# Performance work log

Measured on AMD Instinct MI355X. Metric: run time of the kernel, lower is better.

Reference implementation:

```python
import jax, jax.numpy as jnp
import numpy as np

B, S, E, H = 8, 512, 1024, 16
Dh = E // H
MAX_LEN = 512


def setup_inputs() -> dict:
    key = jax.random.key(0)
    ks = jax.random.split(key, 16)
    std = 1.0 / np.sqrt(E)
    inp = {
        "query": jax.random.normal(ks[0], (B, S, E), jnp.float32),
        "key": jax.random.normal(ks[1], (B, S, E), jnp.float32),
        "value": jax.random.normal(ks[2], (B, S, E), jnp.float32),
        "Wq": jax.random.normal(ks[3], (E, E), jnp.float32) * std,
        "bq": jax.random.normal(ks[4], (E,), jnp.float32) * std,
        "Wk": jax.random.normal(ks[5], (E, E), jnp.float32) * std,
        "bk": jax.random.normal(ks[6], (E,), jnp.float32) * std,
        "Wv": jax.random.normal(ks[7], (E, E), jnp.float32) * std,
        "bv": jax.random.normal(ks[8], (E,), jnp.float32) * std,
        "Wo": jax.random.normal(ks[9], (E, E), jnp.float32) * std,
        "bo": jax.random.normal(ks[10], (E,), jnp.float32) * std,
        "pos": jax.random.normal(ks[11], (MAX_LEN, 1, E), jnp.float32),
    }
    return inp


def reference(query, key, value, Wq, bq, Wk, bk, Wv, bv, Wo, bo, pos):
    b, sq, e = query.shape
    s = min(sq, key.shape[1])  # target_seq_length (static)
    scale = np.sqrt(Dh).astype(np.float32)
    pe = pos[:s, 0, :][None]  # [1, s, E] broadcast over batch
    q = query[:, :s] @ Wq.T + bq + pe
    k = key[:, :s] @ Wk.T + bk + pe
    v = value[:, :s] @ Wv.T + bv + pe
    # [b, s, H, Dh]
    q = q.reshape(b, s, H, Dh)
    k = k.reshape(b, s, H, Dh)
    v = v.reshape(b, s, H, Dh)
    scores = jnp.einsum("bqhd,bkhd->bhqk", q, k) / scale
    attn = jax.nn.softmax(scores, axis=-1)
    wv = jnp.einsum("bhqk,bkhd->bqhd", attn, v).reshape(b, s, e)
    return wv @ Wo.T + bo
```

## Files before the change

kernel.cpp:

```cpp
#include <hip/hip_runtime.h>
#include <hip/hip_bf16.h>

typedef __attribute__((ext_vector_type(8))) short bfx8;
typedef __attribute__((ext_vector_type(4))) float fx4;

static __device__ __forceinline__ short f2bf(float f) {
  union { float f; unsigned u; } v; v.f = f;
  unsigned r = v.u + 0x7fffu + ((v.u >> 16) & 1u);
  return (short)(r >> 16);
}

static __device__ __forceinline__ void gld16(const void* g, void* l) {
  __builtin_amdgcn_global_load_lds(
      (const __attribute__((address_space(1))) void*)g,
      (__attribute__((address_space(3))) void*)l, 16, 0, 0);
}

constexpr int Bz = 8, Sq = 512, Em = 1024, Hn = 16, Dh = 64;
constexpr int Mrows = Bz * Sq;
constexpr size_t NE = (size_t)Mrows * Em;
constexpr size_t WE = (size_t)Em * Em;

__global__ __launch_bounds__(256) void convert_kernel(
    const float* __restrict__ q, const float* __restrict__ k,
    const float* __restrict__ v,
    const float* __restrict__ Wq, const float* __restrict__ Wk,
    const float* __restrict__ Wv, const float* __restrict__ Wo,
    short* __restrict__ qx, short* __restrict__ kx, short* __restrict__ vx,
    short* __restrict__ wqb, short* __restrict__ wkb,
    short* __restrict__ wvb, short* __restrict__ wob)
{
  const int seg = blockIdx.y;
  const float* src; short* dst; size_t n;
  switch (seg) {
    case 0: src = q;  dst = qx;  n = NE; break;
    case 1: src = k;  dst = kx;  n = NE; break;
    case 2: src = v;  dst = vx;  n = NE; break;
    case 3: src = Wq; dst = wqb; n = WE; break;
    case 4: src = Wk; dst = wkb; n = WE; break;
    case 5: src = Wv; dst = wvb; n = WE; break;
    default: src = Wo; dst = wob; n = WE; break;
  }
  const size_t i = ((size_t)blockIdx.x * 256 + threadIdx.x) * 8;
  if (i >= n) return;
  fx4 a = *(const fx4*)(src + i);
  fx4 b = *(const fx4*)(src + i + 4);
  bfx8 o = { f2bf(a[0]), f2bf(a[1]), f2bf(a[2]), f2bf(a[3]),
             f2bf(b[0]), f2bf(b[1]), f2bf(b[2]), f2bf(b[3]) };
  *(bfx8*)(dst + i) = o;
}


__global__ __launch_bounds__(256) void gemm_qkv_bf16(
    const short* __restrict__ qx, const short* __restrict__ kx,
    const short* __restrict__ vx,
    const short* __restrict__ Wqb, const short* __restrict__ Wkb,
    const short* __restrict__ Wvb,
    const float* __restrict__ bq, const float* __restrict__ bk,
    const float* __restrict__ bv,
    const float* __restrict__ pos,
    short* __restrict__ qb, short* __restrict__ kb, short* __restrict__ vb)
{
  __shared__ short As[128 * 32];
  __shared__ short Bs[128 * 32];
  const int z = blockIdx.z;
  const short* A = (z == 0) ? qx : (z == 1) ? kx : vx;
  const short* W = (z == 0) ? Wqb : (z == 1) ? Wkb : Wvb;
  const float* bias = (z == 0) ? bq : (z == 1) ? bk : bv;
  short* dst = (z == 0) ? qb : (z == 1) ? kb : vb;

  const int m0 = blockIdx.x * 128, n0 = blockIdx.y * 128;
  const int t = threadIdx.x, lane = t & 63, wave = t >> 6;
  const int wr = wave >> 1, wc = wave & 1;
  const int fr = lane & 15, fq = lane >> 4;

  const int r0 = t >> 2, o0 = (t & 3) * 8;
  const int r1 = r0 + 64;
  short* lA0 = As + wave * 512;
  short* lA1 = As + 2048 + wave * 512;
  short* lB0 = Bs + wave * 512;
  short* lB1 = Bs + 2048 + wave * 512;

  fx4 acc[4][4] = {};

  for (int k0 = 0; k0 < Em; k0 += 32) {
    gld16(A + (size_t)(m0 + r0) * Em + k0 + o0, lA0);
    gld16(A + (size_t)(m0 + r1) * Em + k0 + o0, lA1);
    gld16(W + (size_t)(n0 + r0) * Em + k0 + o0, lB0);
    gld16(W + (size_t)(n0 + r1) * Em + k0 + o0, lB1);
    __syncthreads();

    bfx8 af[4], bf[4];
#pragma unroll
    for (int m = 0; m < 4; ++m)
      af[m] = *(const bfx8*)&As[(wr * 64 + m * 16 + fr) * 32 + fq * 8];
#pragma unroll
    for (int n = 0; n < 4; ++n)
      bf[n] = *(const bfx8*)&Bs[(wc * 64 + n * 16 + fr) * 32 + fq * 8];
#pragma unroll
    for (int m = 0; m < 4; ++m)
#pragma unroll
      for (int n = 0; n < 4; ++n)
        acc[m][n] = __builtin_amdgcn_mfma_f32_16x16x32_bf16(af[m], bf[n], acc[m][n], 0, 0, 0);
    __syncthreads();
  }

#pragma unroll
  for (int m = 0; m < 4; ++m) {
    const int mm = m0 + wr * 64 + m * 16 + fq * 4;
#pragma unroll
    for (int n = 0; n < 4; ++n) {
      const int nn = n0 + wc * 64 + n * 16 + fr;
      const float bb = bias[nn];
      const int h = nn >> 6, d = nn & 63;
#pragma unroll
      for (int i = 0; i < 4; ++i) {
        const int row = mm + i;
        const int s = row & (Sq - 1), b = row >> 9;
        const float val = acc[m][n][i] + bb + pos[(size_t)s * Em + nn];
        dst[(((size_t)b * Hn + h) * Sq + s) * Dh + d] = f2bf(val);
      }
    }
  }
}

__global__ __launch_bounds__(256) void gemm_out_bf16(
    const short* __restrict__ wv, const short* __restrict__ Wob,
    const float* __restrict__ bo, float* __restrict__ out)
{
  __shared__ short As[128 * 32];
  __shared__ short Bs[128 * 32];

  const int m0 = blockIdx.x * 128, n0 = blockIdx.y * 128;
  const int t = threadIdx.x, lane = t & 63, wave = t >> 6;
  const int wr = wave >> 1, wc = wave & 1;
  const int fr = lane & 15, fq = lane >> 4;

  const int r0 = t >> 2, o0 = (t & 3) * 8;
  const int r1 = r0 + 64;
  short* lA0 = As + wave * 512;
  short* lA1 = As + 2048 + wave * 512;
  short* lB0 = Bs + wave * 512;
  short* lB1 = Bs + 2048 + wave * 512;

  fx4 acc[4][4] = {};

  for (int k0 = 0; k0 < Em; k0 += 32) {
    gld16(wv + (size_t)(m0 + r0) * Em + k0 + o0, lA0);
    gld16(wv + (size_t)(m0 + r1) * Em + k0 + o0, lA1);
    gld16(Wob + (size_t)(n0 + r0) * Em + k0 + o0, lB0);
    gld16(Wob + (size_t)(n0 + r1) * Em + k0 + o0, lB1);
    __syncthreads();

    bfx8 af[4], bf[4];
#pragma unroll
    for (int m = 0; m < 4; ++m)
      af[m] = *(const bfx8*)&As[(wr * 64 + m * 16 + fr) * 32 + fq * 8];
#pragma unroll
    for (int n = 0; n < 4; ++n)
      bf[n] = *(const bfx8*)&Bs[(wc * 64 + n * 16 + fr) * 32 + fq * 8];
#pragma unroll
    for (int m = 0; m < 4; ++m)
#pragma unroll
      for (int n = 0; n < 4; ++n)
        acc[m][n] = __builtin_amdgcn_mfma_f32_16x16x32_bf16(af[m], bf[n], acc[m][n], 0, 0, 0);
    __syncthreads();
  }

#pragma unroll
  for (int m = 0; m < 4; ++m) {
    const int mm = m0 + wr * 64 + m * 16 + fq * 4;
#pragma unroll
    for (int n = 0; n < 4; ++n) {
      const int nn = n0 + wc * 64 + n * 16 + fr;
      const float bb = bo[nn];
#pragma unroll
      for (int i = 0; i < 4; ++i)
        out[(size_t)(mm + i) * Em + nn] = acc[m][n][i] + bb;
    }
  }
}

constexpr int KVB = 64, LDK = 72;

__global__ __launch_bounds__(256) void attn_kernel(
    const short* __restrict__ qb, const short* __restrict__ kb,
    const short* __restrict__ vb, short* __restrict__ wv)
{
  __shared__ short Ks[KVB * LDK];
  __shared__ short Vt[Dh * LDK];
  __shared__ short Ps[4][16 * LDK];

  const int bh = blockIdx.x;
  const int qt = blockIdx.y;
  const int t = threadIdx.x, lane = t & 63, wave = t >> 6;
  const int fr = lane & 15, fq = lane >> 4;

  const size_t base = (size_t)bh * Sq * Dh;
  const int q0 = qt * 64 + wave * 16;

  bfx8 qf[2];
  {
    const short* qp = qb + base + (size_t)(q0 + fr) * Dh;
    qf[0] = *(const bfx8*)(qp + fq * 8);
    qf[1] = *(const bfx8*)(qp + 32 + fq * 8);
  }

  float mrow[4] = { -1e30f, -1e30f, -1e30f, -1e30f };
  float lrow[4] = { 0.f, 0.f, 0.f, 0.f };
  fx4 oacc[4] = {};

  const int kr = t >> 2, kc = (t & 3) * 16;
  const int vr = t & 63, vdb = (t >> 6) * 16;

  for (int kv0 = 0; kv0 < Sq; kv0 += KVB) {
    {
      const short* kp = kb + base + (size_t)(kv0 + kr) * Dh + kc;
      bfx8 u0 = *(const bfx8*)kp;
      bfx8 u1 = *(const bfx8*)(kp + 8);
      *(bfx8*)&Ks[kr * LDK + kc] = u0;
      *(bfx8*)&Ks[kr * LDK + kc + 8] = u1;
    }
    {
      const short* vp = vb + base + (size_t)(kv0 + vr) * Dh + vdb;
      bfx8 u0 = *(const bfx8*)vp;
      bfx8 u1 = *(const bfx8*)(vp + 8);
#pragma unroll
      for (int j = 0; j < 8; ++j) {
        Vt[(vdb + j) * LDK + vr] = u0[j];
        Vt[(vdb + 8 + j) * LDK + vr] = u1[j];
      }
    }
    __syncthreads();

    fx4 sa[4] = {};
#pragma unroll
    for (int nf = 0; nf < 4; ++nf) {
#pragma unroll
      for (int ks = 0; ks < 2; ++ks) {
        bfx8 kf = *(const bfx8*)&Ks[(nf * 16 + fr) * LDK + ks * 32 + fq * 8];
        sa[nf] = __builtin_amdgcn_mfma_f32_16x16x32_bf16(qf[ks], kf, sa[nf], 0, 0, 0);
      }
    }

#pragma unroll
    for (int i = 0; i < 4; ++i) {
      float mx = fmaxf(fmaxf(sa[0][i], sa[1][i]), fmaxf(sa[2][i], sa[3][i]));
      mx = fmaxf(mx, __shfl_xor(mx, 1));
      mx = fmaxf(mx, __shfl_xor(mx, 2));
      mx = fmaxf(mx, __shfl_xor(mx, 4));
      mx = fmaxf(mx, __shfl_xor(mx, 8));
      mx *= 0.125f;
      const float mn = fmaxf(mrow[i], mx);
      const float alpha = __expf(mrow[i] - mn);
      mrow[i] = mn;
      float rs = 0.f;
#pragma unroll
      for (int nf = 0; nf < 4; ++nf) {
        const float p = __expf(sa[nf][i] * 0.125f - mn);
        rs += p;
        Ps[wave][(fq * 4 + i) * LDK + nf * 16 + fr] = f2bf(p);
      }
      rs += __shfl_xor(rs, 1);
      rs += __shfl_xor(rs, 2);
      rs += __shfl_xor(rs, 4);
      rs += __shfl_xor(rs, 8);
      lrow[i] = lrow[i] * alpha + rs;
#pragma unroll
      for (int df = 0; df < 4; ++df) oacc[df][i] *= alpha;
    }
    __syncthreads();

    bfx8 pf[2];
    pf[0] = *(const bfx8*)&Ps[wave][fr * LDK + fq * 8];
    pf[1] = *(const bfx8*)&Ps[wave][fr * LDK + 32 + fq * 8];
#pragma unroll
    for (int df = 0; df < 4; ++df) {
#pragma unroll
      for (int ks = 0; ks < 2; ++ks) {
        bfx8 vf = *(const bfx8*)&Vt[(df * 16 + fr) * LDK + ks * 32 + fq * 8];
        oacc[df] = __builtin_amdgcn_mfma_f32_16x16x32_bf16(pf[ks], vf, oacc[df], 0, 0, 0);
      }
    }
    __syncthreads();
  }

  const int b = bh >> 4, h = bh & 15;
#pragma unroll
  for (int df = 0; df < 4; ++df) {
    const int d = df * 16 + fr;
#pragma unroll
    for (int i = 0; i < 4; ++i) {
      const int qrow = q0 + fq * 4 + i;
      const float o = oacc[df][i] / lrow[i];
      wv[((size_t)b * Sq + qrow) * Em + h * Dh + d] = f2bf(o);
    }
  }
}

extern "C" void kernel_launch(void* const* d_in, const int* in_sizes, int n_in,
                              void* d_out, int out_size, void* d_ws, size_t ws_size,
                              hipStream_t stream) {
  (void)in_sizes; (void)n_in; (void)out_size; (void)ws_size;
  const float* query = (const float*)d_in[0];
  const float* key   = (const float*)d_in[1];
  const float* value = (const float*)d_in[2];
  const float* Wq = (const float*)d_in[3];
  const float* bq = (const float*)d_in[4];
  const float* Wk = (const float*)d_in[5];
  const float* bk = (const float*)d_in[6];
  const float* Wv = (const float*)d_in[7];
  const float* bv = (const float*)d_in[8];
  const float* Wo = (const float*)d_in[9];
  const float* bo = (const float*)d_in[10];
  const float* pos = (const float*)d_in[11];

  short* qx = (short*)d_ws;
  short* kx = qx + NE;
  short* vx = kx + NE;
  short* Wqb = vx + NE;
  short* Wkb = Wqb + WE;
  short* Wvb = Wkb + WE;
  short* Wob = Wvb + WE;
  short* qb = Wob + WE;
  short* wv = qx;
  short* kb = (short*)d_out;
  short* vb = kb + NE;

  convert_kernel<<<dim3(2048, 7), 256, 0, stream>>>(
      query, key, value, Wq, Wk, Wv, Wo, qx, kx, vx, Wqb, Wkb, Wvb, Wob);
  gemm_qkv_bf16<<<dim3(Mrows / 128, Em / 128, 3), 256, 0, stream>>>(
      qx, kx, vx, Wqb, Wkb, Wvb, bq, bk, bv, pos, qb, kb, vb);
  attn_kernel<<<dim3(Bz * Hn, Sq / 64), 256, 0, stream>>>(qb, kb, vb, wv);
  gemm_out_bf16<<<dim3(Mrows / 128, Em / 128), 256, 0, stream>>>(
      wv, Wob, bo, (float*)d_out);
}
```

Baseline: 125.6 us.

## Swap GEMM operand roles for vectorized epilogues and pre-transpose V in projection

```diff
diff --git a/kernel.cpp b/kernel.cpp
--- a/kernel.cpp
+++ b/kernel.cpp
@@ -2,6 +2,7 @@
 #include <hip/hip_bf16.h>
 
 typedef __attribute__((ext_vector_type(8))) short bfx8;
+typedef __attribute__((ext_vector_type(4))) short bfx4;
 typedef __attribute__((ext_vector_type(4))) float fx4;
 
 static __device__ __forceinline__ short f2bf(float f) {
@@ -64,12 +65,13 @@
   __shared__ short As[128 * 32];
   __shared__ short Bs[128 * 32];
   const int z = blockIdx.z;
-  const short* A = (z == 0) ? qx : (z == 1) ? kx : vx;
+  const short* X = (z == 0) ? qx : (z == 1) ? kx : vx;
   const short* W = (z == 0) ? Wqb : (z == 1) ? Wkb : Wvb;
   const float* bias = (z == 0) ? bq : (z == 1) ? bk : bv;
   short* dst = (z == 0) ? qb : (z == 1) ? kb : vb;
 
-  const int m0 = blockIdx.x * 128, n0 = blockIdx.y * 128;
+  const int n0 = blockIdx.x * 128;
+  const int m0 = blockIdx.y * 128;
   const int t = threadIdx.x, lane = t & 63, wave = t >> 6;
   const int wr = wave >> 1, wc = wave & 1;
   const int fr = lane & 15, fq = lane >> 4;
@@ -84,41 +86,47 @@
   fx4 acc[4][4] = {};
 
   for (int k0 = 0; k0 < Em; k0 += 32) {
-    gld16(A + (size_t)(m0 + r0) * Em + k0 + o0, lA0);
-    gld16(A + (size_t)(m0 + r1) * Em + k0 + o0, lA1);
-    gld16(W + (size_t)(n0 + r0) * Em + k0 + o0, lB0);
-    gld16(W + (size_t)(n0 + r1) * Em + k0 + o0, lB1);
+    gld16(W + (size_t)(n0 + r0) * Em + k0 + o0, lA0);
+    gld16(W + (size_t)(n0 + r1) * Em + k0 + o0, lA1);
+    gld16(X + (size_t)(m0 + r0) * Em + k0 + o0, lB0);
+    gld16(X + (size_t)(m0 + r1) * Em + k0 + o0, lB1);
     __syncthreads();
 
     bfx8 af[4], bf[4];
 #pragma unroll
-    for (int m = 0; m < 4; ++m)
-      af[m] = *(const bfx8*)&As[(wr * 64 + m * 16 + fr) * 32 + fq * 8];
-#pragma unroll
-    for (int n = 0; n < 4; ++n)
-      bf[n] = *(const bfx8*)&Bs[(wc * 64 + n * 16 + fr) * 32 + fq * 8];
-#pragma unroll
-    for (int m = 0; m < 4; ++m)
-#pragma unroll
-      for (int n = 0; n < 4; ++n)
-        acc[m][n] = __builtin_amdgcn_mfma_f32_16x16x32_bf16(af[m], bf[n], acc[m][n], 0, 0, 0);
-    __syncthreads();
-  }
-
-#pragma unroll
-  for (int m = 0; m < 4; ++m) {
-    const int mm = m0 + wr * 64 + m * 16 + fq * 4;
-#pragma unroll
-    for (int n = 0; n < 4; ++n) {
-      const int nn = n0 + wc * 64 + n * 16 + fr;
-      const float bb = bias[nn];
-      const int h = nn >> 6, d = nn & 63;
-#pragma unroll
-      for (int i = 0; i < 4; ++i) {
-        const int row = mm + i;
-        const int s = row & (Sq - 1), b = row >> 9;
-        const float val = acc[m][n][i] + bb + pos[(size_t)s * Em + nn];
-        dst[(((size_t)b * Hn + h) * Sq + s) * Dh + d] = f2bf(val);
+    for (int u = 0; u < 4; ++u)
+      af[u] = *(const bfx8*)&As[(wr * 64 + u * 16 + fr) * 32 + fq * 8];
+#pragma unroll
+    for (int v = 0; v < 4; ++v)
+      bf[v] = *(const bfx8*)&Bs[(wc * 64 + v * 16 + fr) * 32 + fq * 8];
+#pragma unroll
+    for (int u = 0; u < 4; ++u)
+#pragma unroll
+      for (int v = 0; v < 4; ++v)
+        acc[u][v] = __builtin_amdgcn_mfma_f32_16x16x32_bf16(af[u], bf[v], acc[u][v], 0, 0, 0);
+    __syncthreads();
+  }
+
+#pragma unroll
+  for (int u = 0; u < 4; ++u) {
+    const int nn = n0 + wr * 64 + u * 16 + fq * 4;
+    const int h = nn >> 6, d = nn & 63;
+    const fx4 bb = *(const fx4*)&bias[nn];
+#pragma unroll
+    for (int v = 0; v < 4; ++v) {
+      const int m = m0 + wc * 64 + v * 16 + fr;
+      const int s = m & (Sq - 1), b = m >> 9;
+      const fx4 pe = *(const fx4*)&pos[(size_t)s * Em + nn];
+      const fx4 a = acc[u][v];
+      if (z < 2) {
+        bfx4 o = { f2bf(a[0] + bb[0] + pe[0]), f2bf(a[1] + bb[1] + pe[1]),
+                   f2bf(a[2] + bb[2] + pe[2]), f2bf(a[3] + bb[3] + pe[3]) };
+        *(bfx4*)&dst[(((size_t)b * Hn + h) * Sq + s) * Dh + d] = o;
+      } else {
+        const size_t tb = ((size_t)b * Hn + h) * Dh;
+#pragma unroll
+        for (int i = 0; i < 4; ++i)
+          dst[(tb + d + i) * Sq + s] = f2bf(a[i] + bb[i] + pe[i]);
       }
     }
   }
@@ -131,7 +139,8 @@
   __shared__ short As[128 * 32];
   __shared__ short Bs[128 * 32];
 
-  const int m0 = blockIdx.x * 128, n0 = blockIdx.y * 128;
+  const int n0 = blockIdx.x * 128;
+  const int m0 = blockIdx.y * 128;
   const int t = threadIdx.x, lane = t & 63, wave = t >> 6;
   const int wr = wave >> 1, wc = wave & 1;
   const int fr = lane & 15, fq = lane >> 4;
@@ -146,37 +155,37 @@
   fx4 acc[4][4] = {};
 
   for (int k0 = 0; k0 < Em; k0 += 32) {
-    gld16(wv + (size_t)(m0 + r0) * Em + k0 + o0, lA0);
-    gld16(wv + (size_t)(m0 + r1) * Em + k0 + o0, lA1);
-    gld16(Wob + (size_t)(n0 + r0) * Em + k0 + o0, lB0);
-    gld16(Wob + (size_t)(n0 + r1) * Em + k0 + o0, lB1);
+    gld16(Wob + (size_t)(n0 + r0) * Em + k0 + o0, lA0);
+    gld16(Wob + (size_t)(n0 + r1) * Em + k0 + o0, lA1);
+    gld16(wv + (size_t)(m0 + r0) * Em + k0 + o0, lB0);
+    gld16(wv + (size_t)(m0 + r1) * Em + k0 + o0, lB1);
     __syncthreads();
 
     bfx8 af[4], bf[4];
 #pragma unroll
-    for (int m = 0; m < 4; ++m)
-      af[m] = *(const bfx8*)&As[(wr * 64 + m * 16 + fr) * 32 + fq * 8];
-#pragma unroll
-    for (int n = 0; n < 4; ++n)
-      bf[n] = *(const bfx8*)&Bs[(wc * 64 + n * 16 + fr) * 32 + fq * 8];
-#pragma unroll
-    for (int m = 0; m < 4; ++m)
-#pragma unroll
-      for (int n = 0; n < 4; ++n)
-        acc[m][n] = __builtin_amdgcn_mfma_f32_16x16x32_bf16(af[m], bf[n], acc[m][n], 0, 0, 0);
-    __syncthreads();
-  }
-
-#pragma unroll
-  for (int m = 0; m < 4; ++m) {
-    const int mm = m0 + wr * 64 + m * 16 + fq * 4;
-#pragma unroll
-    for (int n = 0; n < 4; ++n) {
-      const int nn = n0 + wc * 64 + n * 16 + fr;
-      const float bb = bo[nn];
-#pragma unroll
-      for (int i = 0; i < 4; ++i)
-        out[(size_t)(mm + i) * Em + nn] = acc[m][n][i] + bb;
+    for (int u = 0; u < 4; ++u)
+      af[u] = *(const bfx8*)&As[(wr * 64 + u * 16 + fr) * 32 + fq * 8];
+#pragma unroll
+    for (int v = 0; v < 4; ++v)
+      bf[v] = *(const bfx8*)&Bs[(wc * 64 + v * 16 + fr) * 32 + fq * 8];
+#pragma unroll
+    for (int u = 0; u < 4; ++u)
+#pragma unroll
+      for (int v = 0; v < 4; ++v)
+        acc[u][v] = __builtin_amdgcn_mfma_f32_16x16x32_bf16(af[u], bf[v], acc[u][v], 0, 0, 0);
+    __syncthreads();
+  }
+
+#pragma unroll
+  for (int u = 0; u < 4; ++u) {
+    const int nn = n0 + wr * 64 + u * 16 + fq * 4;
+    const fx4 bb = *(const fx4*)&bo[nn];
+#pragma unroll
+    for (int v = 0; v < 4; ++v) {
+      const int m = m0 + wc * 64 + v * 16 + fr;
+      fx4 val = acc[u][v];
+      val[0] += bb[0]; val[1] += bb[1]; val[2] += bb[2]; val[3] += bb[3];
+      *(fx4*)&out[(size_t)m * Em + nn] = val;
     }
   }
 }
@@ -211,7 +220,6 @@
   fx4 oacc[4] = {};
 
   const int kr = t >> 2, kc = (t & 3) * 16;
-  const int vr = t & 63, vdb = (t >> 6) * 16;
 
   for (int kv0 = 0; kv0 < Sq; kv0 += KVB) {
     {
@@ -222,14 +230,11 @@
       *(bfx8*)&Ks[kr * LDK + kc + 8] = u1;
     }
     {
-      const short* vp = vb + base + (size_t)(kv0 + vr) * Dh + vdb;
+      const short* vp = vb + base + (size_t)kr * Sq + kv0 + kc;
       bfx8 u0 = *(const bfx8*)vp;
       bfx8 u1 = *(const bfx8*)(vp + 8);
-#pragma unroll
-      for (int j = 0; j < 8; ++j) {
-        Vt[(vdb + j) * LDK + vr] = u0[j];
-        Vt[(vdb + 8 + j) * LDK + vr] = u1[j];
-      }
+      *(bfx8*)&Vt[kr * LDK + kc] = u0;
+      *(bfx8*)&Vt[kr * LDK + kc + 8] = u1;
     }
     __syncthreads();
 
@@ -329,9 +334,9 @@
 
   convert_kernel<<<dim3(2048, 7), 256, 0, stream>>>(
       query, key, value, Wq, Wk, Wv, Wo, qx, kx, vx, Wqb, Wkb, Wvb, Wob);
-  gemm_qkv_bf16<<<dim3(Mrows / 128, Em / 128, 3), 256, 0, stream>>>(
+  gemm_qkv_bf16<<<dim3(Em / 128, Mrows / 128, 3), 256, 0, stream>>>(
       qx, kx, vx, Wqb, Wkb, Wvb, bq, bk, bv, pos, qb, kb, vb);
   attn_kernel<<<dim3(Bz * Hn, Sq / 64), 256, 0, stream>>>(qb, kb, vb, wv);
-  gemm_out_bf16<<<dim3(Mrows / 128, Em / 128), 256, 0, stream>>>(
+  gemm_out_bf16<<<dim3(Em / 128, Mrows / 128), 256, 0, stream>>>(
       wv, Wob, bo, (float*)d_out);
 }
```

Result: slower. 134.1 us (+6.7%).
